# Kernel optimization log

Measured on AMD Instinct MI355X. Metric: run time of the kernel, lower is better.

## Reference

```python
import jax, jax.numpy as jnp
import numpy as np

T, B, C, N, H = 4, 32, 384, 196, 12
D = C // H
HID = 1536
ALPHA = 4.0  # spikingjelly default sigmoid surrogate alpha
EPS = 1e-5   # BatchNorm eps
SCALE = 0.25

@jax.custom_vjp
def spike(x):
    return (x >= 0.0).astype(x.dtype)

def _spike_fwd(x):
    return (x >= 0.0).astype(x.dtype), x

def _spike_bwd(x, g):
    s = jax.nn.sigmoid(ALPHA * x)
    return (g * ALPHA * s * (1.0 - s),)

spike.defvjp(_spike_fwd, _spike_bwd)

def lif(x, thr=1.0, tau=2.0):
    # Multi-step LIF, hard reset to 0, detach_reset=True; x: (T, ...)
    def step(v, xt):
        v = v + (xt - v) / tau
        s = spike(v - thr)
        v = v * (1.0 - jax.lax.stop_gradient(s))
        return v, s
    _, out = jax.lax.scan(step, jnp.zeros_like(x[0]), x)
    return out

def conv_bn(x, w, b, g, beta, m, var):
    # 1x1 Conv1d (= channel matmul) + inference-form BatchNorm1d; x: (T,B,Cin,N), w: (Cout,Cin)
    y = jnp.einsum('tbcn,oc->tbon', x, w)
    if b is not None:
        y = y + b[:, None]
    inv = g * jax.lax.rsqrt(var + EPS)
    return y * inv[:, None] + (beta - m * inv)[:, None]

def _heads(t):
    # (T,B,C,N) -> (T,B,H,N,D), matching transpose(-1,-2).reshape(T,B,N,H,D).permute(0,1,3,2,4)
    return jnp.swapaxes(t, -1, -2).reshape(T, B, N, H, D).transpose(0, 1, 3, 2, 4)

def block_fwd(x, policy, wq, qg, qb, qm, qv, wk, kg, kb, km, kvv, wv, vg, vb, vm, vvv,
              wp, bp, pg, pb, pm, pv, w1, b1, g1, be1, m1, v1, w2, b2, g2, be2, m2, v2):
    q = _heads(lif(conv_bn(x, wq, None, qg, qb, qm, qv)))
    k = _heads(lif(conv_bn(x, wk, None, kg, kb, km, kvv)))
    v = _heads(lif(conv_bn(x, wv, None, vg, vb, vm, vvv)))
    attn = jnp.einsum('tbhnd,tbhmd->tbhnm', q, k)           # (T,B,H,N,N)
    pr = policy.reshape(T, B, 1, 1, N)
    eye = jnp.eye(N, dtype=x.dtype)
    attn = attn * (pr + (1.0 - pr) * eye)                   # attention_policy masking
    o = jnp.einsum('tbhnm,tbhmd->tbhnd', attn, v) * SCALE
    o = jnp.swapaxes(o, 3, 4).reshape(T, B, C, N)           # transpose(3,4).reshape(T,B,C,N)
    o = lif(o, thr=0.5)                                     # attn_lif v_threshold=0.5
    o = lif(conv_bn(o, wp, bp, pg, pb, pm, pv))             # proj conv+bn+lif
    x = x + o                                               # residual 1
    h = lif(conv_bn(x, w1, b1, g1, be1, m1, v1))            # MLP fc1
    h = lif(conv_bn(h, w2, b2, g2, be2, m2, v2))            # MLP fc2
    return x + h                                            # residual 2

def setup_inputs():
    key = jax.random.key(0)
    ks = iter(jax.random.split(key, 48))
    def nrm(shape, s=1.0):
        return jax.random.normal(next(ks), shape, jnp.float32) * s
    def uni(shape):
        return jax.random.uniform(next(ks), shape, jnp.float32, minval=0.5, maxval=1.5)
    inp = {}
    inp['x'] = nrm((T, B, C, N))
    inp['policy'] = (jax.random.uniform(next(ks), (T * B, N, 1)) > 0.3).astype(jnp.float32)
    inp.update({'wq': nrm((C, C), 0.05), 'qg': jnp.ones((C,)), 'qb': jnp.zeros((C,)), 'qm': nrm((C,), 0.1), 'qv': uni((C,))})
    inp.update({'wk': nrm((C, C), 0.05), 'kg': jnp.ones((C,)), 'kb': jnp.zeros((C,)), 'km': nrm((C,), 0.1), 'kvv': uni((C,))})
    inp.update({'wv': nrm((C, C), 0.05), 'vg': jnp.ones((C,)), 'vb': jnp.zeros((C,)), 'vm': nrm((C,), 0.1), 'vvv': uni((C,))})
    inp.update({'wp': nrm((C, C), 0.05), 'bp': jnp.zeros((C,)), 'pg': jnp.ones((C,)), 'pb': jnp.zeros((C,)), 'pm': nrm((C,), 0.1), 'pv': uni((C,))})
    inp.update({'w1': nrm((HID, C), 0.05), 'b1': jnp.zeros((HID,)), 'g1': jnp.ones((HID,)), 'be1': jnp.zeros((HID,)), 'm1': nrm((HID,), 0.1), 'v1': uni((HID,))})
    inp.update({'w2': nrm((C, HID), 0.05), 'b2': jnp.zeros((C,)), 'g2': jnp.ones((C,)), 'be2': jnp.zeros((C,)), 'm2': nrm((C,), 0.1), 'v2': uni((C,))})
    return inp

def reference(x, policy, wq, qg, qb, qm, qv, wk, kg, kb, km, kvv, wv, vg, vb, vm, vvv,
              wp, bp, pg, pb, pm, pv, w1, b1, g1, be1, m1, v1, w2, b2, g2, be2, m2, v2):
    return block_fwd(x, policy, wq, qg, qb, qm, qv, wk, kg, kb, km, kvv, wv, vg, vb, vm, vvv,
                     wp, bp, pg, pb, pm, pv, w1, b1, g1, be1, m1, v1, w2, b2, g2, be2, m2, v2)
```

## Files before the change

### kernel.cpp

```cpp
#include <hip/hip_runtime.h>
#include <cstdint>
#include <cstddef>

#define N_POS 196

template<int CIN, bool USE_FMA, bool ACCUM>
__global__ __launch_bounds__(512) void convbn_kernel(
    const float* __restrict__ X, const float* __restrict__ W,
    const float* __restrict__ Bi, const float* __restrict__ Ga,
    const float* __restrict__ Be, const float* __restrict__ Mu,
    const float* __restrict__ Va, float* __restrict__ Y, int Cout,
    int nb, int b0, int xlocal, int ylocal)
{
    __shared__ float Xs[32][200];
    __shared__ float Ws[32][68];
    const int tid = threadIdx.x;
    const int l   = blockIdx.x;
    const int t   = l / nb;
    const int bl  = l - t * nb;
    const int tbg = t * 32 + b0 + bl;
    const int xtb = xlocal ? l : tbg;
    const int ytb = ylocal ? l : tbg;
    const int o0  = blockIdx.y * 64;
    const int n0  = tid & 63;
    const int obase = (tid >> 6) * 8;
    const int col3 = (n0 < 4) ? (n0 + 192) : 196;
    float acc[8][4];
    #pragma unroll
    for (int i = 0; i < 8; ++i)
        #pragma unroll
        for (int j = 0; j < 4; ++j) acc[i][j] = 0.f;
    if (tid < 128) { Xs[tid >> 2][196 + (tid & 3)] = 0.f; }
    const float* Xtb = X + (size_t)xtb * CIN * N_POS;
    const float* Wp  = W + (size_t)o0 * CIN;

    for (int kc = 0; kc < CIN; kc += 32) {
        for (int i = tid; i < 1568; i += 512) {
            int r = i / 49, c4 = i - r * 49;
            *(float4*)&Xs[r][c4 * 4] =
                *(const float4*)(Xtb + (size_t)(kc + r) * N_POS + c4 * 4);
        }
        {
            int oo = tid >> 3, k4 = tid & 7;
            float4 w = *(const float4*)(Wp + (size_t)oo * CIN + kc + k4 * 4);
            Ws[k4 * 4 + 0][oo] = w.x; Ws[k4 * 4 + 1][oo] = w.y;
            Ws[k4 * 4 + 2][oo] = w.z; Ws[k4 * 4 + 3][oo] = w.w;
        }
        __syncthreads();
        #pragma unroll 4
        for (int kk = 0; kk < 32; ++kk) {
            float4 wA = *(const float4*)&Ws[kk][obase];
            float4 wB = *(const float4*)&Ws[kk][obase + 4];
            float xv[4] = { Xs[kk][n0], Xs[kk][n0 + 64], Xs[kk][n0 + 128], Xs[kk][col3] };
            float wv[8] = { wA.x, wA.y, wA.z, wA.w, wB.x, wB.y, wB.z, wB.w };
            #pragma unroll
            for (int i = 0; i < 8; ++i)
                #pragma unroll
                for (int j = 0; j < 4; ++j) {
                    if (USE_FMA) acc[i][j] = fmaf(wv[i], xv[j], acc[i][j]);
                    else         acc[i][j] = __fadd_rn(acc[i][j], __fmul_rn(wv[i], xv[j]));
                }
        }
        __syncthreads();
    }
    #pragma unroll
    for (int i = 0; i < 8; ++i) {
        int o = o0 + obase + i;
        float sc = __fmul_rn(Ga[o], 1.0f / sqrtf(__fadd_rn(Va[o], 1e-5f)));
        float sh = __fsub_rn(Be[o], __fmul_rn(Mu[o], sc));
        float* yp = Y + ((size_t)ytb * Cout + o) * N_POS;
        #pragma unroll
        for (int j = 0; j < 4; ++j) {
            if (j == 3 && n0 >= 4) continue;
            float y = acc[i][j];
            if (Bi) y = __fadd_rn(y, Bi[o]);
            float r = __fadd_rn(__fmul_rn(y, sc), sh);
            int n = n0 + j * 64;
            if (ACCUM) yp[n] = __fadd_rn(yp[n], r);
            else       yp[n] = r;
        }
    }
}

__global__ __launch_bounds__(256) void lif_kernel(float* __restrict__ Y, int plane4, float thr)
{
    int idx = blockIdx.x * 256 + threadIdx.x;
    if (idx >= plane4) return;
    float4* Yp = (float4*)Y;
    float v0 = 0.f, v1 = 0.f, v2 = 0.f, v3 = 0.f;
    #pragma unroll
    for (int t = 0; t < 4; ++t) {
        float4 xv = Yp[(size_t)t * plane4 + idx];
        v0 = __fadd_rn(v0, __fmul_rn(__fsub_rn(xv.x, v0), 0.5f));
        v1 = __fadd_rn(v1, __fmul_rn(__fsub_rn(xv.y, v1), 0.5f));
        v2 = __fadd_rn(v2, __fmul_rn(__fsub_rn(xv.z, v2), 0.5f));
        v3 = __fadd_rn(v3, __fmul_rn(__fsub_rn(xv.w, v3), 0.5f));
        float s0 = (__fsub_rn(v0, thr) >= 0.f) ? 1.f : 0.f;
        float s1 = (__fsub_rn(v1, thr) >= 0.f) ? 1.f : 0.f;
        float s2 = (__fsub_rn(v2, thr) >= 0.f) ? 1.f : 0.f;
        float s3 = (__fsub_rn(v3, thr) >= 0.f) ? 1.f : 0.f;
        v0 = __fmul_rn(v0, 1.f - s0); v1 = __fmul_rn(v1, 1.f - s1);
        v2 = __fmul_rn(v2, 1.f - s2); v3 = __fmul_rn(v3, 1.f - s3);
        xv.x = s0; xv.y = s1; xv.z = s2; xv.w = s3;
        Yp[(size_t)t * plane4 + idx] = xv;
    }
}

__global__ __launch_bounds__(256) void lif_add_kernel(
    const float* __restrict__ Yin, float* __restrict__ Out, int b0)
{
    const int PL4 = 8 * 384 * 49;
    const int B4  = 384 * 49;
    int idx = blockIdx.x * 256 + threadIdx.x;
    if (idx >= PL4) return;
    int bl = idx / B4, r = idx - bl * B4;
    const float4* Yp = (const float4*)Yin;
    float v0 = 0.f, v1 = 0.f, v2 = 0.f, v3 = 0.f;
    #pragma unroll
    for (int t = 0; t < 4; ++t) {
        float4 xv = Yp[(size_t)t * PL4 + idx];
        v0 = __fadd_rn(v0, __fmul_rn(__fsub_rn(xv.x, v0), 0.5f));
        v1 = __fadd_rn(v1, __fmul_rn(__fsub_rn(xv.y, v1), 0.5f));
        v2 = __fadd_rn(v2, __fmul_rn(__fsub_rn(xv.z, v2), 0.5f));
        v3 = __fadd_rn(v3, __fmul_rn(__fsub_rn(xv.w, v3), 0.5f));
        float s0 = (__fsub_rn(v0, 1.0f) >= 0.f) ? 1.f : 0.f;
        float s1 = (__fsub_rn(v1, 1.0f) >= 0.f) ? 1.f : 0.f;
        float s2 = (__fsub_rn(v2, 1.0f) >= 0.f) ? 1.f : 0.f;
        float s3 = (__fsub_rn(v3, 1.0f) >= 0.f) ? 1.f : 0.f;
        v0 = __fmul_rn(v0, 1.f - s0); v1 = __fmul_rn(v1, 1.f - s1);
        v2 = __fmul_rn(v2, 1.f - s2); v3 = __fmul_rn(v3, 1.f - s3);
        float4* op = (float4*)Out + ((size_t)(t * 32 + b0 + bl) * B4 + r);
        float4 o = *op;
        o.x = __fadd_rn(o.x, s0); o.y = __fadd_rn(o.y, s1);
        o.z = __fadd_rn(o.z, s2); o.w = __fadd_rn(o.w, s3);
        *op = o;
    }
}

__global__ __launch_bounds__(256) void pack_kernel(const float* __restrict__ S,
                                                   uint32_t* __restrict__ Bits)
{
    int idx = blockIdx.x * 256 + threadIdx.x;
    if (idx >= 4 * 32 * 12 * 196) return;
    int n = idx % 196;
    int rest = idx / 196;
    int h = rest % 12;
    int tb = rest / 12;
    const float* sp = S + ((size_t)tb * 384 + h * 32) * 196 + n;
    uint32_t bits = 0;
    #pragma unroll
    for (int d = 0; d < 32; ++d)
        bits |= (sp[(size_t)d * 196] > 0.5f) ? (1u << d) : 0u;
    Bits[idx] = bits;
}

__global__ __launch_bounds__(256) void attn_kernel(
    const uint32_t* __restrict__ Qb, const uint32_t* __restrict__ Kb,
    const float* __restrict__ V, const float* __restrict__ P, float* __restrict__ O)
{
    __shared__ uint32_t Qbs[196], Kbs[196];
    __shared__ float Ps[196];
    __shared__ float Vs[32][204];
    __shared__ float Ss[32][204];
    __shared__ float Os[32][36];
    const int tid = threadIdx.x;
    const int bid = blockIdx.x;
    const int tb = bid / 12, h = bid - tb * 12;
    const size_t vbase = ((size_t)tb * 384 + h * 32) * 196;
    const size_t qbase = ((size_t)tb * 12 + h) * 196;
    for (int i = tid; i < 196; i += 256) {
        Qbs[i] = Qb[qbase + i];
        Kbs[i] = Kb[qbase + i];
        Ps[i]  = P[(size_t)tb * 196 + i];
    }
    for (int i = tid; i < 32 * 49; i += 256) {
        int d = i / 49, m4 = i - d * 49;
        *(float4*)&Vs[d][m4 * 4] = *(const float4*)(V + vbase + (size_t)d * 196 + m4 * 4);
    }
    __syncthreads();
    for (int n0 = 0; n0 < 196; n0 += 32) {
        const int rows = min(32, 196 - n0);
        for (int idx = tid; idx < rows * 196; idx += 256) {
            int ns = idx / 196, m = idx - ns * 196;
            int n = n0 + ns;
            float s = (float)__popc(Qbs[n] & Kbs[m]);
            float p = Ps[m];
            float e = (m == n) ? 1.f : 0.f;
            Ss[ns][m] = s * (p + (1.f - p) * e);
        }
        __syncthreads();
        {
            const int tn = tid & 15, td = tid >> 4;
            float a00 = 0, a01 = 0, a10 = 0, a11 = 0;
            #pragma unroll 7
            for (int m4 = 0; m4 < 49; ++m4) {
                float4 s0 = *(const float4*)&Ss[tn][m4 * 4];
                float4 s1 = *(const float4*)&Ss[tn + 16][m4 * 4];
                float4 u0 = *(const float4*)&Vs[td][m4 * 4];
                float4 u1 = *(const float4*)&Vs[td + 16][m4 * 4];
                a00 += s0.x * u0.x + s0.y * u0.y + s0.z * u0.z + s0.w * u0.w;
                a01 += s0.x * u1.x + s0.y * u1.y + s0.z * u1.z + s0.w * u1.w;
                a10 += s1.x * u0.x + s1.y * u0.y + s1.z * u0.z + s1.w * u0.w;
                a11 += s1.x * u1.x + s1.y * u1.y + s1.z * u1.z + s1.w * u1.w;
            }
            Os[td     ][tn     ] = a00 * 0.25f;
            Os[td + 16][tn     ] = a01 * 0.25f;
            Os[td     ][tn + 16] = a10 * 0.25f;
            Os[td + 16][tn + 16] = a11 * 0.25f;
        }
        __syncthreads();
        {
            const int d = tid >> 3, c4 = tid & 7;
            if (c4 * 4 < rows)
                *(float4*)(O + vbase + (size_t)d * 196 + n0 + c4 * 4) =
                    *(const float4*)&Os[d][c4 * 4];
        }
        __syncthreads();
    }
}

__global__ __launch_bounds__(256) void add_kernel(const float* __restrict__ A,
    const float* __restrict__ B, float* __restrict__ Out, int n4)
{
    int idx = blockIdx.x * 256 + threadIdx.x;
    if (idx >= n4) return;
    float4 a = ((const float4*)A)[idx];
    float4 b = ((const float4*)B)[idx];
    float4 o;
    o.x = __fadd_rn(a.x, b.x); o.y = __fadd_rn(a.y, b.y);
    o.z = __fadd_rn(a.z, b.z); o.w = __fadd_rn(a.w, b.w);
    ((float4*)Out)[idx] = o;
}

extern "C" void kernel_launch(void* const* d_in, const int* in_sizes, int n_in,
                              void* d_out, int out_size, void* d_ws, size_t ws_size,
                              hipStream_t stream) {
    const float* x   = (const float*)d_in[0];
    const float* pol = (const float*)d_in[1];
    const float* wq = (const float*)d_in[2];
    const float* qg = (const float*)d_in[3];
    const float* qb = (const float*)d_in[4];
    const float* qm = (const float*)d_in[5];
    const float* qv = (const float*)d_in[6];
    const float* wk = (const float*)d_in[7];
    const float* kg = (const float*)d_in[8];
    const float* kb = (const float*)d_in[9];
    const float* km = (const float*)d_in[10];
    const float* kvv= (const float*)d_in[11];
    const float* wv = (const float*)d_in[12];
    const float* vg = (const float*)d_in[13];
    const float* vb = (const float*)d_in[14];
    const float* vm = (const float*)d_in[15];
    const float* vvv= (const float*)d_in[16];
    const float* wp = (const float*)d_in[17];
    const float* bp = (const float*)d_in[18];
    const float* pg = (const float*)d_in[19];
    const float* pb = (const float*)d_in[20];
    const float* pm = (const float*)d_in[21];
    const float* pv = (const float*)d_in[22];
    const float* w1 = (const float*)d_in[23];
    const float* b1 = (const float*)d_in[24];
    const float* g1 = (const float*)d_in[25];
    const float* be1= (const float*)d_in[26];
    const float* m1 = (const float*)d_in[27];
    const float* v1 = (const float*)d_in[28];
    const float* w2 = (const float*)d_in[29];
    const float* b2 = (const float*)d_in[30];
    const float* g2 = (const float*)d_in[31];
    const float* be2= (const float*)d_in[32];
    const float* m2 = (const float*)d_in[33];
    const float* v2 = (const float*)d_in[34];

    float* bufA = (float*)d_ws;
    float* bufD = bufA + 9633792;
    uint32_t* Qbits = (uint32_t*)(bufD + 2408448);
    uint32_t* Kbits = Qbits + 301056;
    float* out = (float*)d_out;

    convbn_kernel<384, false, false><<<dim3(128, 6), 512, 0, stream>>>(x, wq, nullptr, qg, qb, qm, qv, bufA, 384, 32, 0, 0, 0);
    lif_kernel<<<2352, 256, 0, stream>>>(bufA, 602112, 1.0f);
    pack_kernel<<<1176, 256, 0, stream>>>(bufA, Qbits);
    convbn_kernel<384, false, false><<<dim3(128, 6), 512, 0, stream>>>(x, wk, nullptr, kg, kb, km, kvv, bufA, 384, 32, 0, 0, 0);
    lif_kernel<<<2352, 256, 0, stream>>>(bufA, 602112, 1.0f);
    pack_kernel<<<1176, 256, 0, stream>>>(bufA, Kbits);
    convbn_kernel<384, false, false><<<dim3(128, 6), 512, 0, stream>>>(x, wv, nullptr, vg, vb, vm, vvv, bufA, 384, 32, 0, 0, 0);
    lif_kernel<<<2352, 256, 0, stream>>>(bufA, 602112, 1.0f);

    attn_kernel<<<1536, 256, 0, stream>>>(Qbits, Kbits, bufA, pol, out);
    lif_kernel<<<2352, 256, 0, stream>>>(out, 602112, 0.5f);

    convbn_kernel<384, true, false><<<dim3(128, 6), 512, 0, stream>>>(out, wp, bp, pg, pb, pm, pv, bufA, 384, 32, 0, 0, 0);
    lif_kernel<<<2352, 256, 0, stream>>>(bufA, 602112, 1.0f);
    add_kernel<<<9408, 256, 0, stream>>>(x, bufA, out, 2408448);

    for (int c = 0; c < 4; ++c) {
        convbn_kernel<384, false, false><<<dim3(32, 24), 512, 0, stream>>>(out, w1, b1, g1, be1, m1, v1, bufA, 1536, 8, c * 8, 0, 1);
        lif_kernel<<<2352, 256, 0, stream>>>(bufA, 602112, 1.0f);
        convbn_kernel<1536, true, false><<<dim3(32, 6), 512, 0, stream>>>(bufA, w2, b2, g2, be2, m2, v2, bufD, 384, 8, c * 8, 1, 1);
        lif_add_kernel<<<588, 256, 0, stream>>>(bufD, out, c * 8);
    }
}
```

Before: 2.284 ms.

## Double-buffer conv tiles with async global-to-LDS loads

The conv+BN matmul kernel now stages its input tiles straight into LDS with global_load_lds, in 16-channel chunks across two buffers. The next chunk is loaded while the current one is computed, which removes the load-then-sync stall of the old 32-channel single-buffer loop. Weights are transposed into LDS through registers as before. The cost is twice as many barriers per reduction, and correctness depends on the barrier waiting for the async LDS writes to finish. The zero padding past column 196 is also dropped, so the unused fourth column now reads neighbouring data that is then discarded.

```diff
diff --git a/kernel.cpp b/kernel.cpp
--- a/kernel.cpp
+++ b/kernel.cpp
@@ -3,6 +3,13 @@
 #include <cstddef>
 
 #define N_POS 196
+
+__device__ __forceinline__ void async_copy16(const float* g, float* l) {
+    __builtin_amdgcn_global_load_lds(
+        (const __attribute__((address_space(1))) uint32_t*)g,
+        (__attribute__((address_space(3))) uint32_t*)l,
+        16, 0, 0);
+}
 
 template<int CIN, bool USE_FMA, bool ACCUM>
 __global__ __launch_bounds__(512) void convbn_kernel(
@@ -12,8 +19,10 @@
     const float* __restrict__ Va, float* __restrict__ Y, int Cout,
     int nb, int b0, int xlocal, int ylocal)
 {
-    __shared__ float Xs[32][200];
-    __shared__ float Ws[32][68];
+    constexpr int NCH = CIN / 16;
+    __shared__ float lds[2 * 3136 + 2 * 1024];
+    float* Xs = lds;
+    float* Ws = lds + 6272;
     const int tid = threadIdx.x;
     const int l   = blockIdx.x;
     const int t   = l / nb;
@@ -25,33 +34,46 @@
     const int n0  = tid & 63;
     const int obase = (tid >> 6) * 8;
     const int col3 = (n0 < 4) ? (n0 + 192) : 196;
+    const float* Xtb = X + (size_t)xtb * CIN * N_POS;
+    const float* Wp  = W + (size_t)o0 * CIN;
+
     float acc[8][4];
     #pragma unroll
     for (int i = 0; i < 8; ++i)
         #pragma unroll
         for (int j = 0; j < 4; ++j) acc[i][j] = 0.f;
-    if (tid < 128) { Xs[tid >> 2][196 + (tid & 3)] = 0.f; }
-    const float* Xtb = X + (size_t)xtb * CIN * N_POS;
-    const float* Wp  = W + (size_t)o0 * CIN;
-
-    for (int kc = 0; kc < CIN; kc += 32) {
-        for (int i = tid; i < 1568; i += 512) {
-            int r = i / 49, c4 = i - r * 49;
-            *(float4*)&Xs[r][c4 * 4] =
-                *(const float4*)(Xtb + (size_t)(kc + r) * N_POS + c4 * 4);
-        }
+
+    auto stage = [&](int buf, int kc) {
+        const int oo = tid >> 3, k2 = (tid & 7) * 2;
+        float2 wv2 = *(const float2*)(Wp + (size_t)oo * CIN + kc + k2);
         {
-            int oo = tid >> 3, k4 = tid & 7;
-            float4 w = *(const float4*)(Wp + (size_t)oo * CIN + kc + k4 * 4);
-            Ws[k4 * 4 + 0][oo] = w.x; Ws[k4 * 4 + 1][oo] = w.y;
-            Ws[k4 * 4 + 2][oo] = w.z; Ws[k4 * 4 + 3][oo] = w.w;
-        }
-        __syncthreads();
+            int i = tid;
+            const float* g = Xtb + (size_t)(kc + i / 49) * N_POS + (i % 49) * 4;
+            async_copy16(g, &Xs[buf * 3136 + (i & ~63) * 4]);
+        }
+        if (tid < 272) {
+            int i = tid + 512;
+            const float* g = Xtb + (size_t)(kc + i / 49) * N_POS + (i % 49) * 4;
+            async_copy16(g, &Xs[buf * 3136 + (i & ~63) * 4]);
+        }
+        Ws[buf * 1024 + k2 * 64 + oo]       = wv2.x;
+        Ws[buf * 1024 + (k2 + 1) * 64 + oo] = wv2.y;
+    };
+
+    stage(0, 0);
+    __syncthreads();
+
+    int buf = 0;
+    for (int ch = 0; ch < NCH; ++ch) {
+        if (ch + 1 < NCH) stage(buf ^ 1, (ch + 1) * 16);
+        const float* Xb = Xs + buf * 3136;
+        const float* Wb = Ws + buf * 1024;
         #pragma unroll 4
-        for (int kk = 0; kk < 32; ++kk) {
-            float4 wA = *(const float4*)&Ws[kk][obase];
-            float4 wB = *(const float4*)&Ws[kk][obase + 4];
-            float xv[4] = { Xs[kk][n0], Xs[kk][n0 + 64], Xs[kk][n0 + 128], Xs[kk][col3] };
+        for (int kk = 0; kk < 16; ++kk) {
+            float4 wA = *(const float4*)(Wb + kk * 64 + obase);
+            float4 wB = *(const float4*)(Wb + kk * 64 + obase + 4);
+            float xv[4] = { Xb[kk * 196 + n0], Xb[kk * 196 + n0 + 64],
+                            Xb[kk * 196 + n0 + 128], Xb[kk * 196 + col3] };
             float wv[8] = { wA.x, wA.y, wA.z, wA.w, wB.x, wB.y, wB.z, wB.w };
             #pragma unroll
             for (int i = 0; i < 8; ++i)
@@ -62,7 +84,9 @@
                 }
         }
         __syncthreads();
-    }
+        buf ^= 1;
+    }
+
     #pragma unroll
     for (int i = 0; i < 8; ++i) {
         int o = o0 + obase + i;
```

New measurement: 2.249 ms. About the same (-1.5%).
